# Optimization experiments

Hardware: AMD Instinct MI355X
Metric: run time of the kernel (lower is better)

## Reference

```python
import jax, jax.numpy as jnp
import numpy as np

B, HW, NTGT, C = 2, 4096, 4096, 512
H, KNN = 8, 32
DH = C // H
SCALE = DH ** -0.5


def setup_inputs() -> dict:
    key = jax.random.key(0)
    ks = jax.random.split(key, 12)
    s = 1.0 / np.sqrt(C)
    return {
        "src": jax.random.normal(ks[0], (B, HW, C), jnp.float32),
        "tgt": jax.random.normal(ks[1], (B, NTGT, C), jnp.float32),
        "indices": jax.random.randint(ks[2], (B, HW, KNN), 0, NTGT, jnp.int64),
        "weights": jax.random.normal(ks[3], (B, HW, KNN), jnp.float32),
        "Wq": jax.random.normal(ks[4], (C, C), jnp.float32) * s,
        "bq": jnp.zeros((C,), jnp.float32),
        "Wk": jax.random.normal(ks[5], (C, C), jnp.float32) * s,
        "bk": jnp.zeros((C,), jnp.float32),
        "Wv": jax.random.normal(ks[6], (C, C), jnp.float32) * s,
        "bv": jnp.zeros((C,), jnp.float32),
        "Wo": jax.random.normal(ks[7], (C, C), jnp.float32) * s,
        "bo": jnp.zeros((C,), jnp.float32),
    }


def reference(src, tgt, indices, weights, Wq, bq, Wk, bk, Wv, bv, Wo, bo):
    b, hw, c = src.shape
    # projections -> (b, H, seq, dh)
    q = (src @ Wq + bq).reshape(b, hw, H, DH).transpose(0, 2, 1, 3)
    k = (tgt @ Wk + bk).reshape(b, -1, H, DH).transpose(0, 2, 1, 3)
    v = (tgt @ Wv + bv).reshape(b, -1, H, DH).transpose(0, 2, 1, 3)
    # gather epipolar neighbors: per batch, kb[:, idx] -> (H, hw, KNN, dh)
    gather = jax.vmap(lambda xb, ib: xb[:, ib])
    k_g = gather(k, indices)  # (b, H, hw, KNN, dh)
    v_g = gather(v, indices)  # (b, H, hw, KNN, dh)
    logits = jnp.einsum("bhqd,bhqkd->bhqk", q, k_g) * SCALE
    logits = logits + weights[:, None]  # broadcast over heads
    attn = jax.nn.softmax(logits, axis=-1)
    out = jnp.einsum("bhqk,bhqkd->bhqd", attn, v_g)
    out = out.transpose(0, 2, 1, 3).reshape(b, hw, c)
    return out @ Wo + bo
```

## Files before the change

### kernel.cpp

```cpp
#include <hip/hip_runtime.h>
#include <hip/hip_bf16.h>
#include <stdint.h>
#include <type_traits>

#define B_    2
#define HW_   4096
#define NTGT_ 4096
#define C_    512
#define H_    8
#define KNN_  32
#define DH_   64
#define M_    (B_ * HW_)

typedef unsigned short ushort_t;
typedef _Float16 f16x8 __attribute__((ext_vector_type(8)));
typedef __fp16 hf2 __attribute__((ext_vector_type(2)));
typedef float floatx4 __attribute__((ext_vector_type(4)));

__device__ __forceinline__ uint32_t pkh(float x, float y) {
    union { hf2 h; uint32_t u; } c;
    c.h = __builtin_amdgcn_cvt_pkrtz(x, y);
    return c.u;
}
__device__ __forceinline__ ushort_t f2h(float f) {
    return (ushort_t)(pkh(f, 0.f) & 0xffffu);
}
__device__ __forceinline__ float h2f(ushort_t u) {
    union { ushort_t s; __fp16 h; } x;
    x.s = u;
    return (float)x.h;
}
__device__ __forceinline__ ushort_t f2b(float f) {
    union { float f; uint32_t i; } x;
    x.f = f;
    uint32_t r = x.i + 0x7fffu + ((x.i >> 16) & 1u);
    return (ushort_t)(r >> 16);
}
__device__ __forceinline__ float dot2acc(uint32_t a, uint32_t b, float c) {
#if __has_builtin(__builtin_amdgcn_fdot2)
    union { uint32_t u; hf2 h; } xa, xb;
    xa.u = a; xb.u = b;
    return __builtin_amdgcn_fdot2(xa.h, xb.h, c, false);
#else
    c = fmaf(h2f((ushort_t)(a & 0xffffu)), h2f((ushort_t)(b & 0xffffu)), c);
    return fmaf(h2f((ushort_t)(a >> 16)), h2f((ushort_t)(b >> 16)), c);
#endif
}
__device__ __forceinline__ uint4 pack8(const float4& a, const float4& b) {
    return make_uint4(pkh(a.x, a.y), pkh(a.z, a.w), pkh(b.x, b.y), pkh(b.z, b.w));
}

__global__ __launch_bounds__(256) void transpose_cvt4(
    const float* __restrict__ W0, const float* __restrict__ W1,
    const float* __restrict__ W2, const float* __restrict__ W3,
    ushort_t* __restrict__ T0, ushort_t* __restrict__ T1,
    ushort_t* __restrict__ T2, ushort_t* __restrict__ T3) {
    __shared__ float tile[32][33];

    const float* W = (blockIdx.z == 0) ? W0 : (blockIdx.z == 1) ? W1
                     : (blockIdx.z == 2) ? W2 : W3;
    ushort_t* T = (blockIdx.z == 0) ? T0 : (blockIdx.z == 1) ? T1
                  : (blockIdx.z == 2) ? T2 : T3;

    const int k0 = blockIdx.x * 32;
    const int n0 = blockIdx.y * 32;
    const int t = threadIdx.x;
    const int r = t >> 3;
    const int c0 = (t & 7) * 4;

    float4 d = *(const float4*)&W[(size_t)(k0 + r) * 512 + n0 + c0];
    tile[r][c0 + 0] = d.x; tile[r][c0 + 1] = d.y;
    tile[r][c0 + 2] = d.z; tile[r][c0 + 3] = d.w;
    __syncthreads();

    uint2 o;
    o.x = pkh(tile[c0 + 0][r], tile[c0 + 1][r]);
    o.y = pkh(tile[c0 + 2][r], tile[c0 + 3][r]);
    *(uint2*)&T[(size_t)(n0 + r) * 512 + k0 + c0] = o;
}

__global__ __launch_bounds__(256) void transpose_inplace4_f32(
    float* W0, float* W1, float* W2, float* W3) {
    __shared__ float ta[32][33];
    __shared__ float tb[32][33];

    float* W = (blockIdx.y == 0) ? W0 : (blockIdx.y == 1) ? W1
               : (blockIdx.y == 2) ? W2 : W3;

    int p = blockIdx.x;
    int i = 0, acc = 0;
    while (acc + (16 - i) <= p) { acc += 16 - i; ++i; }
    const int j = i + (p - acc);

    const int t = threadIdx.x;
    const int r = t >> 3;
    const int c0 = (t & 7) * 4;

    {
        float4 d = *(const float4*)&W[(size_t)(i * 32 + r) * 512 + j * 32 + c0];
        ta[r][c0 + 0] = d.x; ta[r][c0 + 1] = d.y;
        ta[r][c0 + 2] = d.z; ta[r][c0 + 3] = d.w;
    }
    if (i != j) {
        float4 d = *(const float4*)&W[(size_t)(j * 32 + r) * 512 + i * 32 + c0];
        tb[r][c0 + 0] = d.x; tb[r][c0 + 1] = d.y;
        tb[r][c0 + 2] = d.z; tb[r][c0 + 3] = d.w;
    }
    __syncthreads();

    *(float4*)&W[(size_t)(j * 32 + r) * 512 + i * 32 + c0] =
        make_float4(ta[c0 + 0][r], ta[c0 + 1][r], ta[c0 + 2][r], ta[c0 + 3][r]);
    if (i != j)
        *(float4*)&W[(size_t)(i * 32 + r) * 512 + j * 32 + c0] =
            make_float4(tb[c0 + 0][r], tb[c0 + 1][r], tb[c0 + 2][r], tb[c0 + 3][r]);
}

template <typename AT, typename BT, typename OT, int BN, bool OBF16>
__device__ __forceinline__ void gemm_body(const AT* __restrict__ A,
                                          const BT* __restrict__ Wt,
                                          const float* __restrict__ bias,
                                          OT* __restrict__ O,
                                          int bm, int bn) {
    constexpr int NJ = BN / 32;
    __shared__ ushort_t As[128][40];
    __shared__ ushort_t Bs[BN][40];

    const int t = threadIdx.x;
    const int lr = t >> 2;
    const int lc = (t & 3) * 8;

    const int lane = t & 63;
    const int wv = t >> 6;
    const int wr = (wv >> 1) * 64;
    const int wc = (wv & 1) * (BN / 2);
    const int r16 = lane & 15;
    const int quad = lane >> 4;

    floatx4 acc[4][NJ] = {};

    float4 fa0, fa1, fa2, fa3, fb0, fb1, fb2, fb3;
    uint4 ua0, ua1, ub0, ub1;

    if constexpr (std::is_same<AT, float>::value) {
        const float* p0 = &A[(size_t)(bm + lr) * 512 + lc];
        const float* p1 = &A[(size_t)(bm + lr + 64) * 512 + lc];
        fa0 = *(const float4*)p0; fa1 = *(const float4*)(p0 + 4);
        fa2 = *(const float4*)p1; fa3 = *(const float4*)(p1 + 4);
    } else {
        ua0 = *(const uint4*)&A[(size_t)(bm + lr) * 512 + lc];
        ua1 = *(const uint4*)&A[(size_t)(bm + lr + 64) * 512 + lc];
    }
    if constexpr (std::is_same<BT, float>::value) {
        const float* p0 = &Wt[(size_t)(bn + lr) * 512 + lc];
        fb0 = *(const float4*)p0; fb1 = *(const float4*)(p0 + 4);
        if constexpr (BN == 128) {
            const float* p1 = &Wt[(size_t)(bn + lr + 64) * 512 + lc];
            fb2 = *(const float4*)p1; fb3 = *(const float4*)(p1 + 4);
        }
    } else {
        ub0 = *(const uint4*)&Wt[(size_t)(bn + lr) * 512 + lc];
        if constexpr (BN == 128)
            ub1 = *(const uint4*)&Wt[(size_t)(bn + lr + 64) * 512 + lc];
    }

    for (int kt = 0; kt < 512; kt += 32) {
        __syncthreads();
        if constexpr (std::is_same<AT, float>::value) {
            *(uint4*)&As[lr][lc] = pack8(fa0, fa1);
            *(uint4*)&As[lr + 64][lc] = pack8(fa2, fa3);
        } else {
            *(uint4*)&As[lr][lc] = ua0;
            *(uint4*)&As[lr + 64][lc] = ua1;
        }
        if constexpr (std::is_same<BT, float>::value) {
            *(uint4*)&Bs[lr][lc] = pack8(fb0, fb1);
            if constexpr (BN == 128) *(uint4*)&Bs[lr + 64][lc] = pack8(fb2, fb3);
        } else {
            *(uint4*)&Bs[lr][lc] = ub0;
            if constexpr (BN == 128) *(uint4*)&Bs[lr + 64][lc] = ub1;
        }
        __syncthreads();

        if (kt + 32 < 512) {
            const int k2 = kt + 32;
            if constexpr (std::is_same<AT, float>::value) {
                const float* p0 = &A[(size_t)(bm + lr) * 512 + k2 + lc];
                const float* p1 = &A[(size_t)(bm + lr + 64) * 512 + k2 + lc];
                fa0 = *(const float4*)p0; fa1 = *(const float4*)(p0 + 4);
                fa2 = *(const float4*)p1; fa3 = *(const float4*)(p1 + 4);
            } else {
                ua0 = *(const uint4*)&A[(size_t)(bm + lr) * 512 + k2 + lc];
                ua1 = *(const uint4*)&A[(size_t)(bm + lr + 64) * 512 + k2 + lc];
            }
            if constexpr (std::is_same<BT, float>::value) {
                const float* p0 = &Wt[(size_t)(bn + lr) * 512 + k2 + lc];
                fb0 = *(const float4*)p0; fb1 = *(const float4*)(p0 + 4);
                if constexpr (BN == 128) {
                    const float* p1 = &Wt[(size_t)(bn + lr + 64) * 512 + k2 + lc];
                    fb2 = *(const float4*)p1; fb3 = *(const float4*)(p1 + 4);
                }
            } else {
                ub0 = *(const uint4*)&Wt[(size_t)(bn + lr) * 512 + k2 + lc];
                if constexpr (BN == 128)
                    ub1 = *(const uint4*)&Wt[(size_t)(bn + lr + 64) * 512 + k2 + lc];
            }
        }

        f16x8 af[4], bf[NJ];
#pragma unroll
        for (int i = 0; i < 4; ++i)
            af[i] = *(const f16x8*)&As[wr + i * 16 + r16][quad * 8];
#pragma unroll
        for (int j = 0; j < NJ; ++j)
            bf[j] = *(const f16x8*)&Bs[wc + j * 16 + r16][quad * 8];
#pragma unroll
        for (int i = 0; i < 4; ++i)
#pragma unroll
            for (int j = 0; j < NJ; ++j)
                acc[i][j] = __builtin_amdgcn_mfma_f32_16x16x32_f16(
                    af[i], bf[j], acc[i][j], 0, 0, 0);
    }

#pragma unroll
    for (int j = 0; j < NJ; ++j) {
        const int col = bn + wc + j * 16 + r16;
        const float bj = bias[col];
#pragma unroll
        for (int i = 0; i < 4; ++i) {
            const int row = bm + wr + i * 16 + quad * 4;
#pragma unroll
            for (int r = 0; r < 4; ++r) {
                float v = acc[i][j][r] + bj;
                if constexpr (std::is_same<OT, float>::value)
                    O[(size_t)(row + r) * 512 + col] = v;
                else if constexpr (OBF16)
                    O[(size_t)(row + r) * 512 + col] = f2b(v);
                else
                    O[(size_t)(row + r) * 512 + col] = f2h(v);
            }
        }
    }
}

template <typename BT>
__global__ __launch_bounds__(256, 3) void gemm_qkv(
    const float* __restrict__ src, const float* __restrict__ tgt,
    const BT* __restrict__ WtQ, const BT* __restrict__ WtK,
    const BT* __restrict__ WtV,
    const float* __restrict__ bq, const float* __restrict__ bk,
    const float* __restrict__ bv,
    ushort_t* __restrict__ Qb, ushort_t* __restrict__ Kb,
    ushort_t* __restrict__ Vb) {
    const int id = blockIdx.x;
    const int xcd = id & 7;
    const int g = id >> 3;
    const int mgrp = g / 12;
    const int r = g % 12;
    const int z = r >> 2;
    const int bn = (r & 3) * 128;
    const int bm = (xcd + 8 * mgrp) * 128;

    const float* A = (z == 0) ? src : tgt;
    const BT* Wt = (z == 0) ? WtQ : (z == 1) ? WtK : WtV;
    const float* bias = (z == 0) ? bq : (z == 1) ? bk : bv;
    ushort_t* O = (z == 0) ? Qb : (z == 1) ? Kb : Vb;
    gemm_body<float, BT, ushort_t, 128, false>(A, Wt, bias, O, bm, bn);
}

template <typename BT, typename OT, bool OBF16>
__global__ __launch_bounds__(256, 4) void gemm_o(const ushort_t* __restrict__ A,
                                                 const BT* __restrict__ Wt,
                                                 const float* __restrict__ bias,
                                                 OT* __restrict__ O) {
    const int id = blockIdx.x;
    const int xcd = id & 7;
    const int g = id >> 3;
    const int mgrp = g >> 3;
    const int bn = (g & 7) * 64;
    const int bm = (xcd + 8 * mgrp) * 128;
    gemm_body<ushort_t, BT, OT, 64, OBF16>(A, Wt, bias, O, bm, bn);
}

#define KVSTRIDE 520
template <typename IT>
__global__ __launch_bounds__(256, 7) void attn_kernel(
    const ushort_t* __restrict__ Q, const ushort_t* __restrict__ K,
    const ushort_t* __restrict__ V, const IT* __restrict__ idx,
    const float* __restrict__ wts, ushort_t* O) {
    __shared__ ushort_t kvs[16][KVSTRIDE];
    __shared__ float ps[H_][KNN_];

    const int t = threadIdx.x;
    const int id = blockIdx.x;
    const int xcd = id & 7;
    const int slot = id >> 3;
    const int bt = xcd >> 2;
    const int bq = bt * HW_ + (xcd & 3) * 1024 + slot;
    const size_t qoff = (size_t)bq * C_;

    const int h = t >> 5;
    const int l5 = t & 31;
    const int nl = l5 & 15;
    const int half = l5 >> 4;
    const int koff = h * 64 + half * 32;
    const int prow = t >> 4;
    const int pcol = (t & 15) * 8;

    const IT* ibp = idx + (size_t)bq * KNN_;
    const int i0 = (int)ibp[prow];
    const int i1 = (int)ibp[prow + 16];
    const float w0 = wts[(size_t)bq * KNN_ + nl];
    const float w1 = wts[(size_t)bq * KNN_ + nl + 16];
    const ushort_t* qp = Q + qoff + koff;
    const uint4 q0 = *(const uint4*)(qp);
    const uint4 q1 = *(const uint4*)(qp + 8);
    const uint4 q2 = *(const uint4*)(qp + 16);
    const uint4 q3 = *(const uint4*)(qp + 24);

    const ushort_t* Kbase = K + (size_t)bt * NTGT_ * C_;
    const ushort_t* Vbase = V + (size_t)bt * NTGT_ * C_;

    uint4 a0, a1, a2, a3, b0, b1, b2, b3;
    {
        const ushort_t* p = Kbase + (size_t)i0 * C_ + pcol;
        a0 = *(const uint4*)(p);       a1 = *(const uint4*)(p + 128);
        a2 = *(const uint4*)(p + 256); a3 = *(const uint4*)(p + 384);
    }
    {
        const ushort_t* p = Kbase + (size_t)i1 * C_ + pcol;
        b0 = *(const uint4*)(p);       b1 = *(const uint4*)(p + 128);
        b2 = *(const uint4*)(p + 256); b3 = *(const uint4*)(p + 384);
    }
    *(uint4*)&kvs[prow][pcol + 0]   = a0;
    *(uint4*)&kvs[prow][pcol + 128] = a1;
    *(uint4*)&kvs[prow][pcol + 256] = a2;
    *(uint4*)&kvs[prow][pcol + 384] = a3;
    {
        const ushort_t* p = Vbase + (size_t)i0 * C_ + pcol;
        a0 = *(const uint4*)(p);       a1 = *(const uint4*)(p + 128);
        a2 = *(const uint4*)(p + 256); a3 = *(const uint4*)(p + 384);
    }
    __syncthreads();

    float l0, l1;
    {
        uint4 kv0 = *(const uint4*)&kvs[nl][koff + 0];
        uint4 kv1 = *(const uint4*)&kvs[nl][koff + 8];
        uint4 kv2 = *(const uint4*)&kvs[nl][koff + 16];
        uint4 kv3 = *(const uint4*)&kvs[nl][koff + 24];
        float da = 0.f, db = 0.f;
        da = dot2acc(kv0.x, q0.x, da); da = dot2acc(kv0.y, q0.y, da);
        da = dot2acc(kv0.z, q0.z, da); da = dot2acc(kv0.w, q0.w, da);
        db = dot2acc(kv1.x, q1.x, db); db = dot2acc(kv1.y, q1.y, db);
        db = dot2acc(kv1.z, q1.z, db); db = dot2acc(kv1.w, q1.w, db);
        da = dot2acc(kv2.x, q2.x, da); da = dot2acc(kv2.y, q2.y, da);
        da = dot2acc(kv2.z, q2.z, da); da = dot2acc(kv2.w, q2.w, da);
        db = dot2acc(kv3.x, q3.x, db); db = dot2acc(kv3.y, q3.y, db);
        db = dot2acc(kv3.z, q3.z, db); db = dot2acc(kv3.w, q3.w, db);
        float dot = da + db;
        dot += __shfl_xor(dot, 16);
        l0 = dot * 0.125f + w0;
    }
    __syncthreads();
    *(uint4*)&kvs[prow][pcol + 0]   = b0;
    *(uint4*)&kvs[prow][pcol + 128] = b1;
    *(uint4*)&kvs[prow][pcol + 256] = b2;
    *(uint4*)&kvs[prow][pcol + 384] = b3;
    {
        const ushort_t* p = Vbase + (size_t)i1 * C_ + pcol;
        b0 = *(const uint4*)(p);       b1 = *(const uint4*)(p + 128);
        b2 = *(const uint4*)(p + 256); b3 = *(const uint4*)(p + 384);
    }
    __syncthreads();
    {
        uint4 kv0 = *(const uint4*)&kvs[nl][koff + 0];
        uint4 kv1 = *(const uint4*)&kvs[nl][koff + 8];
        uint4 kv2 = *(const uint4*)&kvs[nl][koff + 16];
        uint4 kv3 = *(const uint4*)&kvs[nl][koff + 24];
        float da = 0.f, db = 0.f;
        da = dot2acc(kv0.x, q0.x, da); da = dot2acc(kv0.y, q0.y, da);
        da = dot2acc(kv0.z, q0.z, da); da = dot2acc(kv0.w, q0.w, da);
        db = dot2acc(kv1.x, q1.x, db); db = dot2acc(kv1.y, q1.y, db);
        db = dot2acc(kv1.z, q1.z, db); db = dot2acc(kv1.w, q1.w, db);
        da = dot2acc(kv2.x, q2.x, da); da = dot2acc(kv2.y, q2.y, da);
        da = dot2acc(kv2.z, q2.z, da); da = dot2acc(kv2.w, q2.w, da);
        db = dot2acc(kv3.x, q3.x, db); db = dot2acc(kv3.y, q3.y, db);
        db = dot2acc(kv3.z, q3.z, db); db = dot2acc(kv3.w, q3.w, db);
        float dot = da + db;
        dot += __shfl_xor(dot, 16);
        l1 = dot * 0.125f + w1;
    }
    {
        float m = fmaxf(l0, l1);
#pragma unroll
        for (int o = 16; o > 0; o >>= 1) m = fmaxf(m, __shfl_xor(m, o));
        float e0 = __expf(l0 - m), e1 = __expf(l1 - m);
        float s = e0 + e1;
#pragma unroll
        for (int o = 16; o > 0; o >>= 1) s += __shfl_xor(s, o);
        const float inv = 2.0f / s;
        ps[h][nl] = e0 * inv;
        ps[h][nl + 16] = e1 * inv;
    }
    __syncthreads();
    *(uint4*)&kvs[prow][pcol + 0]   = a0;
    *(uint4*)&kvs[prow][pcol + 128] = a1;
    *(uint4*)&kvs[prow][pcol + 256] = a2;
    *(uint4*)&kvs[prow][pcol + 384] = a3;
    __syncthreads();

    const int d2 = l5 * 2;
    float f0 = 0.f, f1 = 0.f;
#pragma unroll
    for (int nn = 0; nn < 16; ++nn) {
        uint32_t vv = *(const uint32_t*)&kvs[nn][h * DH_ + d2];
        float p = ps[h][nn];
        f0 = fmaf(p, h2f((ushort_t)(vv & 0xffffu)), f0);
        f1 = fmaf(p, h2f((ushort_t)(vv >> 16)), f1);
    }
    __syncthreads();
    *(uint4*)&kvs[prow][pcol + 0]   = b0;
    *(uint4*)&kvs[prow][pcol + 128] = b1;
    *(uint4*)&kvs[prow][pcol + 256] = b2;
    *(uint4*)&kvs[prow][pcol + 384] = b3;
    __syncthreads();
#pragma unroll
    for (int nn = 0; nn < 16; ++nn) {
        uint32_t vv = *(const uint32_t*)&kvs[nn][h * DH_ + d2];
        float p = ps[h][nn + 16];
        f0 = fmaf(p, h2f((ushort_t)(vv & 0xffffu)), f0);
        f1 = fmaf(p, h2f((ushort_t)(vv >> 16)), f1);
    }
    *(uint32_t*)(O + qoff + h * DH_ + d2) = pkh(f0, f1);
}

static int elem_bytes(const void* p, size_t n, int dflt) {
    size_t sz = 0;
    hipError_t err = hipPointerGetAttribute(
        &sz, HIP_POINTER_ATTRIBUTE_RANGE_SIZE, (hipDeviceptr_t)(uintptr_t)p);
    if (err == hipSuccess && sz >= n && (sz % n) == 0) {
        size_t b = sz / n;
        if (b == 2 || b == 4 || b == 8) return (int)b;
    }
    return dflt;
}

extern "C" void kernel_launch(void* const* d_in, const int* in_sizes, int n_in,
                              void* d_out, int out_size, void* d_ws, size_t ws_size,
                              hipStream_t stream) {
    const float* src  = (const float*)d_in[0];
    const float* tgt  = (const float*)d_in[1];
    const void*  idxp = d_in[2];
    const float* wtp  = (const float*)d_in[3];
    float* Wq = (float*)d_in[4];  const float* bq = (const float*)d_in[5];
    float* Wk = (float*)d_in[6];  const float* bk = (const float*)d_in[7];
    float* Wv = (float*)d_in[8];  const float* bv = (const float*)d_in[9];
    float* Wo = (float*)d_in[10]; const float* bo = (const float*)d_in[11];

    const size_t NELEM = (size_t)M_ * C_;
    const size_t WELEM = (size_t)C_ * C_;
    const size_t NIDX  = (size_t)B_ * HW_ * KNN_;

    const int ib = elem_bytes(idxp, NIDX, 4);
    const int ob = elem_bytes(d_out, NELEM, 4);

    dim3 blk(256);

    ushort_t* Qb = (ushort_t*)d_ws;
    ushort_t* Kb = Qb + NELEM;
    ushort_t* Vb = (ushort_t*)d_out;
    ushort_t* Ob = Qb;

    const bool wfit = ws_size >= (2 * NELEM + 4 * WELEM) * sizeof(ushort_t);

    if (wfit) {
        ushort_t* T = Kb + NELEM;
        ushort_t* WtQ = T;
        ushort_t* WtK = T + WELEM;
        ushort_t* WtV = T + 2 * WELEM;
        ushort_t* WtO = T + 3 * WELEM;

        transpose_cvt4<<<dim3(16, 16, 4), blk, 0, stream>>>(
            Wq, Wk, Wv, Wo, WtQ, WtK, WtV, WtO);

        gemm_qkv<ushort_t><<<dim3(768), blk, 0, stream>>>(
            src, tgt, WtQ, WtK, WtV, bq, bk, bv, Qb, Kb, Vb);

        if (ib == 8)
            attn_kernel<long long><<<dim3(B_ * HW_), blk, 0, stream>>>(
                Qb, Kb, Vb, (const long long*)idxp, wtp, Ob);
        else
            attn_kernel<int><<<dim3(B_ * HW_), blk, 0, stream>>>(
                Qb, Kb, Vb, (const int*)idxp, wtp, Ob);

        if (ob == 2)
            gemm_o<ushort_t, ushort_t, true><<<dim3(512), blk, 0, stream>>>(
                Ob, WtO, bo, (ushort_t*)d_out);
        else
            gemm_o<ushort_t, float, false><<<dim3(512), blk, 0, stream>>>(
                Ob, WtO, bo, (float*)d_out);
    } else {
        transpose_inplace4_f32<<<dim3(136, 4), blk, 0, stream>>>(Wq, Wk, Wv, Wo);

        gemm_qkv<float><<<dim3(768), blk, 0, stream>>>(
            src, tgt, Wq, Wk, Wv, bq, bk, bv, Qb, Kb, Vb);

        if (ib == 8)
            attn_kernel<long long><<<dim3(B_ * HW_), blk, 0, stream>>>(
                Qb, Kb, Vb, (const long long*)idxp, wtp, Ob);
        else
            attn_kernel<int><<<dim3(B_ * HW_), blk, 0, stream>>>(
                Qb, Kb, Vb, (const int*)idxp, wtp, Ob);

        if (ob == 2)
            gemm_o<float, ushort_t, true><<<dim3(512), blk, 0, stream>>>(
                Ob, Wo, bo, (ushort_t*)d_out);
        else
            gemm_o<float, float, false><<<dim3(512), blk, 0, stream>>>(
                Ob, Wo, bo, (float*)d_out);
    }
}
```

Baseline: 190.3 us.

## Split attention into separate QK-softmax and PV kernels

```diff
diff --git a/kernel.cpp b/kernel.cpp
--- a/kernel.cpp
+++ b/kernel.cpp
@@ -283,138 +283,138 @@
 
 #define KVSTRIDE 520
 template <typename IT>
-__global__ __launch_bounds__(256, 7) void attn_kernel(
+__global__ __launch_bounds__(256, 6) void attn_qk(
     const ushort_t* __restrict__ Q, const ushort_t* __restrict__ K,
-    const ushort_t* __restrict__ V, const IT* __restrict__ idx,
-    const float* __restrict__ wts, ushort_t* O) {
-    __shared__ ushort_t kvs[16][KVSTRIDE];
-    __shared__ float ps[H_][KNN_];
-
+    const IT* __restrict__ idx, const float* __restrict__ wts,
+    float* __restrict__ P) {
     const int t = threadIdx.x;
     const int id = blockIdx.x;
     const int xcd = id & 7;
     const int slot = id >> 3;
     const int bt = xcd >> 2;
     const int bq = bt * HW_ + (xcd & 3) * 1024 + slot;
-    const size_t qoff = (size_t)bq * C_;
 
     const int h = t >> 5;
     const int l5 = t & 31;
     const int nl = l5 & 15;
     const int half = l5 >> 4;
     const int koff = h * 64 + half * 32;
-    const int prow = t >> 4;
-    const int pcol = (t & 15) * 8;
 
     const IT* ibp = idx + (size_t)bq * KNN_;
-    const int i0 = (int)ibp[prow];
-    const int i1 = (int)ibp[prow + 16];
+    const int i0 = (int)ibp[nl];
+    const int i1 = (int)ibp[nl + 16];
     const float w0 = wts[(size_t)bq * KNN_ + nl];
     const float w1 = wts[(size_t)bq * KNN_ + nl + 16];
-    const ushort_t* qp = Q + qoff + koff;
+
+    const ushort_t* qp = Q + (size_t)bq * C_ + koff;
     const uint4 q0 = *(const uint4*)(qp);
     const uint4 q1 = *(const uint4*)(qp + 8);
     const uint4 q2 = *(const uint4*)(qp + 16);
     const uint4 q3 = *(const uint4*)(qp + 24);
 
     const ushort_t* Kbase = K + (size_t)bt * NTGT_ * C_;
+    const ushort_t* k0p = Kbase + (size_t)i0 * C_ + koff;
+    const ushort_t* k1p = Kbase + (size_t)i1 * C_ + koff;
+    const uint4 a0 = *(const uint4*)(k0p);      const uint4 a1 = *(const uint4*)(k0p + 8);
+    const uint4 a2 = *(const uint4*)(k0p + 16); const uint4 a3 = *(const uint4*)(k0p + 24);
+    const uint4 b0 = *(const uint4*)(k1p);      const uint4 b1 = *(const uint4*)(k1p + 8);
+    const uint4 b2 = *(const uint4*)(k1p + 16); const uint4 b3 = *(const uint4*)(k1p + 24);
+
+    float l0, l1;
+    {
+        float da = 0.f, db = 0.f;
+        da = dot2acc(a0.x, q0.x, da); da = dot2acc(a0.y, q0.y, da);
+        da = dot2acc(a0.z, q0.z, da); da = dot2acc(a0.w, q0.w, da);
+        db = dot2acc(a1.x, q1.x, db); db = dot2acc(a1.y, q1.y, db);
+        db = dot2acc(a1.z, q1.z, db); db = dot2acc(a1.w, q1.w, db);
+        da = dot2acc(a2.x, q2.x, da); da = dot2acc(a2.y, q2.y, da);
+        da = dot2acc(a2.z, q2.z, da); da = dot2acc(a2.w, q2.w, da);
+        db = dot2acc(a3.x, q3.x, db); db = dot2acc(a3.y, q3.y, db);
+        db = dot2acc(a3.z, q3.z, db); db = dot2acc(a3.w, q3.w, db);
+        float dot = da + db;
+        dot += __shfl_xor(dot, 16);
+        l0 = dot * 0.125f + w0;
+    }
+    {
+        float da = 0.f, db = 0.f;
+        da = dot2acc(b0.x, q0.x, da); da = dot2acc(b0.y, q0.y, da);
+        da = dot2acc(b0.z, q0.z, da); da = dot2acc(b0.w, q0.w, da);
+        db = dot2acc(b1.x, q1.x, db); db = dot2acc(b1.y, q1.y, db);
+        db = dot2acc(b1.z, q1.z, db); db = dot2acc(b1.w, q1.w, db);
+        da = dot2acc(b2.x, q2.x, da); da = dot2acc(b2.y, q2.y, da);
+        da = dot2acc(b2.z, q2.z, da); da = dot2acc(b2.w, q2.w, da);
+        db = dot2acc(b3.x, q3.x, db); db = dot2acc(b3.y, q3.y, db);
+        db = dot2acc(b3.z, q3.z, db); db = dot2acc(b3.w, q3.w, db);
+        float dot = da + db;
+        dot += __shfl_xor(dot, 16);
+        l1 = dot * 0.125f + w1;
+    }
+    float m = fmaxf(l0, l1);
+#pragma unroll
+    for (int o = 16; o > 0; o >>= 1) m = fmaxf(m, __shfl_xor(m, o));
+    float e0 = __expf(l0 - m), e1 = __expf(l1 - m);
+    float s = e0 + e1;
+#pragma unroll
+    for (int o = 16; o > 0; o >>= 1) s += __shfl_xor(s, o);
+    const float inv = 2.0f / s;
+
+    __syncthreads();
+    if (half == 0) {
+        float* pr = P + (size_t)bq * 256 + h * 32 + nl;
+        pr[0] = e0 * inv;
+        pr[16] = e1 * inv;
+    }
+}
+
+template <typename IT>
+__global__ __launch_bounds__(256, 6) void attn_pv(
+    const float* __restrict__ P, const ushort_t* __restrict__ V,
+    const IT* __restrict__ idx, ushort_t* __restrict__ O) {
+    __shared__ ushort_t kvs[16][KVSTRIDE];
+    __shared__ float psh[H_][KNN_];
+
+    const int t = threadIdx.x;
+    const int id = blockIdx.x;
+    const int xcd = id & 7;
+    const int slot = id >> 3;
+    const int bt = xcd >> 2;
+    const int bq = bt * HW_ + (xcd & 3) * 1024 + slot;
+
+    const int h = t >> 5;
+    const int l5 = t & 31;
+    const int d2 = l5 * 2;
+    const int prow = t >> 4;
+    const int pcol = (t & 15) * 8;
+
+    const IT* ibp = idx + (size_t)bq * KNN_;
+    const int i0 = (int)ibp[prow];
+    const int i1 = (int)ibp[prow + 16];
+    const float pv = P[(size_t)bq * 256 + t];
+
     const ushort_t* Vbase = V + (size_t)bt * NTGT_ * C_;
-
     uint4 a0, a1, a2, a3, b0, b1, b2, b3;
-    {
-        const ushort_t* p = Kbase + (size_t)i0 * C_ + pcol;
-        a0 = *(const uint4*)(p);       a1 = *(const uint4*)(p + 128);
-        a2 = *(const uint4*)(p + 256); a3 = *(const uint4*)(p + 384);
-    }
-    {
-        const ushort_t* p = Kbase + (size_t)i1 * C_ + pcol;
-        b0 = *(const uint4*)(p);       b1 = *(const uint4*)(p + 128);
-        b2 = *(const uint4*)(p + 256); b3 = *(const uint4*)(p + 384);
-    }
-    *(uint4*)&kvs[prow][pcol + 0]   = a0;
-    *(uint4*)&kvs[prow][pcol + 128] = a1;
-    *(uint4*)&kvs[prow][pcol + 256] = a2;
-    *(uint4*)&kvs[prow][pcol + 384] = a3;
     {
         const ushort_t* p = Vbase + (size_t)i0 * C_ + pcol;
         a0 = *(const uint4*)(p);       a1 = *(const uint4*)(p + 128);
         a2 = *(const uint4*)(p + 256); a3 = *(const uint4*)(p + 384);
     }
-    __syncthreads();
-
-    float l0, l1;
-    {
-        uint4 kv0 = *(const uint4*)&kvs[nl][koff + 0];
-        uint4 kv1 = *(const uint4*)&kvs[nl][koff + 8];
-        uint4 kv2 = *(const uint4*)&kvs[nl][koff + 16];
-        uint4 kv3 = *(const uint4*)&kvs[nl][koff + 24];
-        float da = 0.f, db = 0.f;
-        da = dot2acc(kv0.x, q0.x, da); da = dot2acc(kv0.y, q0.y, da);
-        da = dot2acc(kv0.z, q0.z, da); da = dot2acc(kv0.w, q0.w, da);
-        db = dot2acc(kv1.x, q1.x, db); db = dot2acc(kv1.y, q1.y, db);
-        db = dot2acc(kv1.z, q1.z, db); db = dot2acc(kv1.w, q1.w, db);
-        da = dot2acc(kv2.x, q2.x, da); da = dot2acc(kv2.y, q2.y, da);
-        da = dot2acc(kv2.z, q2.z, da); da = dot2acc(kv2.w, q2.w, da);
-        db = dot2acc(kv3.x, q3.x, db); db = dot2acc(kv3.y, q3.y, db);
-        db = dot2acc(kv3.z, q3.z, db); db = dot2acc(kv3.w, q3.w, db);
-        float dot = da + db;
-        dot += __shfl_xor(dot, 16);
-        l0 = dot * 0.125f + w0;
-    }
-    __syncthreads();
-    *(uint4*)&kvs[prow][pcol + 0]   = b0;
-    *(uint4*)&kvs[prow][pcol + 128] = b1;
-    *(uint4*)&kvs[prow][pcol + 256] = b2;
-    *(uint4*)&kvs[prow][pcol + 384] = b3;
     {
         const ushort_t* p = Vbase + (size_t)i1 * C_ + pcol;
         b0 = *(const uint4*)(p);       b1 = *(const uint4*)(p + 128);
         b2 = *(const uint4*)(p + 256); b3 = *(const uint4*)(p + 384);
     }
-    __syncthreads();
-    {
-        uint4 kv0 = *(const uint4*)&kvs[nl][koff + 0];
-        uint4 kv1 = *(const uint4*)&kvs[nl][koff + 8];
-        uint4 kv2 = *(const uint4*)&kvs[nl][koff + 16];
-        uint4 kv3 = *(const uint4*)&kvs[nl][koff + 24];
-        float da = 0.f, db = 0.f;
-        da = dot2acc(kv0.x, q0.x, da); da = dot2acc(kv0.y, q0.y, da);
-        da = dot2acc(kv0.z, q0.z, da); da = dot2acc(kv0.w, q0.w, da);
-        db = dot2acc(kv1.x, q1.x, db); db = dot2acc(kv1.y, q1.y, db);
-        db = dot2acc(kv1.z, q1.z, db); db = dot2acc(kv1.w, q1.w, db);
-        da = dot2acc(kv2.x, q2.x, da); da = dot2acc(kv2.y, q2.y, da);
-        da = dot2acc(kv2.z, q2.z, da); da = dot2acc(kv2.w, q2.w, da);
-        db = dot2acc(kv3.x, q3.x, db); db = dot2acc(kv3.y, q3.y, db);
-        db = dot2acc(kv3.z, q3.z, db); db = dot2acc(kv3.w, q3.w, db);
-        float dot = da + db;
-        dot += __shfl_xor(dot, 16);
-        l1 = dot * 0.125f + w1;
-    }
-    {
-        float m = fmaxf(l0, l1);
-#pragma unroll
-        for (int o = 16; o > 0; o >>= 1) m = fmaxf(m, __shfl_xor(m, o));
-        float e0 = __expf(l0 - m), e1 = __expf(l1 - m);
-        float s = e0 + e1;
-#pragma unroll
-        for (int o = 16; o > 0; o >>= 1) s += __shfl_xor(s, o);
-        const float inv = 2.0f / s;
-        ps[h][nl] = e0 * inv;
-        ps[h][nl + 16] = e1 * inv;
-    }
-    __syncthreads();
+    psh[t >> 5][t & 31] = pv;
     *(uint4*)&kvs[prow][pcol + 0]   = a0;
     *(uint4*)&kvs[prow][pcol + 128] = a1;
     *(uint4*)&kvs[prow][pcol + 256] = a2;
     *(uint4*)&kvs[prow][pcol + 384] = a3;
     __syncthreads();
 
-    const int d2 = l5 * 2;
     float f0 = 0.f, f1 = 0.f;
 #pragma unroll
     for (int nn = 0; nn < 16; ++nn) {
         uint32_t vv = *(const uint32_t*)&kvs[nn][h * DH_ + d2];
-        float p = ps[h][nn];
+        float p = psh[h][nn];
         f0 = fmaf(p, h2f((ushort_t)(vv & 0xffffu)), f0);
         f1 = fmaf(p, h2f((ushort_t)(vv >> 16)), f1);
     }
@@ -427,11 +427,11 @@
 #pragma unroll
     for (int nn = 0; nn < 16; ++nn) {
         uint32_t vv = *(const uint32_t*)&kvs[nn][h * DH_ + d2];
-        float p = ps[h][nn + 16];
+        float p = psh[h][nn + 16];
         f0 = fmaf(p, h2f((ushort_t)(vv & 0xffffu)), f0);
         f1 = fmaf(p, h2f((ushort_t)(vv >> 16)), f1);
     }
-    *(uint32_t*)(O + qoff + h * DH_ + d2) = pkh(f0, f1);
+    *(uint32_t*)(O + (size_t)bq * C_ + h * DH_ + d2) = pkh(f0, f1);
 }
 
 static int elem_bytes(const void* p, size_t n, int dflt) {
@@ -469,7 +469,8 @@
     ushort_t* Qb = (ushort_t*)d_ws;
     ushort_t* Kb = Qb + NELEM;
     ushort_t* Vb = (ushort_t*)d_out;
-    ushort_t* Ob = Qb;
+    float* Pb = (float*)Qb;
+    ushort_t* Ob = Kb;
 
     const bool wfit = ws_size >= (2 * NELEM + 4 * WELEM) * sizeof(ushort_t);
 
@@ -486,12 +487,17 @@
         gemm_qkv<ushort_t><<<dim3(768), blk, 0, stream>>>(
             src, tgt, WtQ, WtK, WtV, bq, bk, bv, Qb, Kb, Vb);
 
-        if (ib == 8)
-            attn_kernel<long long><<<dim3(B_ * HW_), blk, 0, stream>>>(
-                Qb, Kb, Vb, (const long long*)idxp, wtp, Ob);
-        else
-            attn_kernel<int><<<dim3(B_ * HW_), blk, 0, stream>>>(
-                Qb, Kb, Vb, (const int*)idxp, wtp, Ob);
+        if (ib == 8) {
+            attn_qk<long long><<<dim3(B_ * HW_), blk, 0, stream>>>(
+                Qb, Kb, (const long long*)idxp, wtp, Pb);
+            attn_pv<long long><<<dim3(B_ * HW_), blk, 0, stream>>>(
+                Pb, Vb, (const long long*)idxp, Ob);
+        } else {
+            attn_qk<int><<<dim3(B_ * HW_), blk, 0, stream>>>(
+                Qb, Kb, (const int*)idxp, wtp, Pb);
+            attn_pv<int><<<dim3(B_ * HW_), blk, 0, stream>>>(
+                Pb, Vb, (const int*)idxp, Ob);
+        }
 
         if (ob == 2)
             gemm_o<ushort_t, ushort_t, true><<<dim3(512), blk, 0, stream>>>(
@@ -505,12 +511,17 @@
         gemm_qkv<float><<<dim3(768), blk, 0, stream>>>(
             src, tgt, Wq, Wk, Wv, bq, bk, bv, Qb, Kb, Vb);
 
-        if (ib == 8)
-            attn_kernel<long long><<<dim3(B_ * HW_), blk, 0, stream>>>(
-                Qb, Kb, Vb, (const long long*)idxp, wtp, Ob);
-        else
-            attn_kernel<int><<<dim3(B_ * HW_), blk, 0, stream>>>(
-                Qb, Kb, Vb, (const int*)idxp, wtp, Ob);
+        if (ib == 8) {
+            attn_qk<long long><<<dim3(B_ * HW_), blk, 0, stream>>>(
+                Qb, Kb, (const long long*)idxp, wtp, Pb);
+            attn_pv<long long><<<dim3(B_ * HW_), blk, 0, stream>>>(
+                Pb, Vb, (const long long*)idxp, Ob);
+        } else {
+            attn_qk<int><<<dim3(B_ * HW_), blk, 0, stream>>>(
+                Qb, Kb, (const int*)idxp, wtp, Pb);
+            attn_pv<int><<<dim3(B_ * HW_), blk, 0, stream>>>(
+                Pb, Vb, (const int*)idxp, Ob);
+        }
 
         if (ob == 2)
             gemm_o<float, ushort_t, true><<<dim3(512), blk, 0, stream>>>(
```

Result: no change. 192.7 us (+1.2%).
